# Performance work log

Measured on AMD Instinct MI355X. Metric: run time of the kernel, lower is better.

The kernel has to match this reference:

```python
import jax, jax.numpy as jnp
import numpy as np

SOFTCAP = 15.0
EPS_RMS = 1e-6
EPS_L2 = 1e-12


def rms_norm(x):
    # F.rms_norm without affine weight
    return x * jax.lax.rsqrt(jnp.mean(x * x, axis=-1, keepdims=True) + EPS_RMS)


def l2_normalize(x):
    # F.normalize(dim=-1): x / max(||x||, eps)
    n = jnp.sqrt(jnp.sum(x * x, axis=-1, keepdims=True))
    return x / jnp.maximum(n, EPS_L2)


def setup_inputs() -> dict:
    key = jax.random.key(0)
    ks = jax.random.split(key, 7)
    B, D, H, KVH, HD = 2, 1024, 16, 4, 64
    chunk_start_idx, chunk_len, n_scratchpad = 2048, 2048, 64
    T = chunk_start_idx + chunk_len + n_scratchpad  # 4160
    s = 0.02
    return {
        "x": jax.random.normal(ks[0], (B, T, D), dtype=jnp.float32),
        "Wq": jax.random.normal(ks[1], (D, D), dtype=jnp.float32) * s,
        "Wk": jax.random.normal(ks[2], (KVH * HD, D), dtype=jnp.float32) * s,
        "Wv": jax.random.normal(ks[3], (KVH * HD, D), dtype=jnp.float32) * s,
        "Wo": jax.random.normal(ks[4], (D, D), dtype=jnp.float32) * s,
        "Wfc": jax.random.normal(ks[5], (4 * D, D), dtype=jnp.float32) * s,
        "Wproj": jax.random.normal(ks[6], (D, 4 * D), dtype=jnp.float32) * s,
        "chunk_start_idx": chunk_start_idx,
        "chunk_len": chunk_len,
        "n_scratchpad": n_scratchpad,
    }


def reference(x, Wq, Wk, Wv, Wo, Wfc, Wproj, chunk_start_idx, chunk_len, n_scratchpad):
    B, T, D = x.shape
    H = 16
    KVH = Wk.shape[0] // (D // H)
    HD = D // H
    update_start = chunk_start_idx
    n_update = T - update_start

    x_norm = rms_norm(x)
    x_upd = x_norm[:, update_start:]

    q = (x_upd @ Wq.T).reshape(B, n_update, H, HD).transpose(0, 2, 1, 3)   # [B,H,Q,hd]
    k = (x_norm @ Wk.T).reshape(B, T, KVH, HD).transpose(0, 2, 1, 3)       # [B,KVH,T,hd]
    v = (x_norm @ Wv.T).reshape(B, T, KVH, HD).transpose(0, 2, 1, 3)

    q = l2_normalize(q)
    k = l2_normalize(k)

    if KVH < H:
        rep = H // KVH
        k = jnp.repeat(k, rep, axis=1)
        v = jnp.repeat(v, rep, axis=1)

    scale = 1.0 / jnp.sqrt(jnp.float32(HD))
    scores = jnp.einsum("bhqd,bhkd->bhqk", q, k) * scale
    q_pos = jnp.arange(update_start, T)[:, None]
    kv_pos = jnp.arange(T)[None, :]
    mask = kv_pos <= q_pos  # [Q,T] causal
    scores = jnp.where(mask[None, None], scores, -jnp.inf)
    probs = jax.nn.softmax(scores, axis=-1)
    attn = jnp.einsum("bhqk,bhkd->bhqd", probs, v)             # [B,H,Q,hd]
    attn = attn.transpose(0, 2, 1, 3).reshape(B, n_update, D)

    attn_out = attn @ Wo.T
    attn_out = SOFTCAP * jnp.tanh(attn_out / SOFTCAP)

    x_new = x[:, update_start:] + attn_out
    h = rms_norm(x_new) @ Wfc.T
    h = jnp.square(jax.nn.relu(h))  # nanochat MLP: relu(x)^2
    x_new = x_new + h @ Wproj.T

    if update_start > 0:
        return jnp.concatenate([x[:, :update_start], x_new], axis=1)
    return x_new
```

## Files before the change

kernel.cpp:

```cpp
#include <hip/hip_runtime.h>
#include <hip/hip_bf16.h>

#define B_   2
#define T_   4160
#define D_   1024
#define H_   16
#define KVH_ 4
#define HD_  64
#define UPD  2048
#define NU   2112
#define MQ   (B_*NU)
#define MT   (B_*T_)

typedef unsigned short u16;
typedef unsigned int u32;
typedef __attribute__((ext_vector_type(8))) short bf16x8;
typedef __attribute__((ext_vector_type(4))) float f32x4;
typedef __attribute__((ext_vector_type(4))) unsigned short u16x4;

__device__ __forceinline__ float bf2f(u16 u){ return __uint_as_float(((unsigned)u)<<16); }
__device__ __forceinline__ u16 f2bf(float f){
  unsigned u = __float_as_uint(f);
  u += 0x7FFF + ((u>>16)&1);
  return (u16)(u>>16);
}

__device__ __forceinline__ void gll16(const void* g, void* l){
  __builtin_amdgcn_global_load_lds((const __attribute__((address_space(1))) char*)g,
                                   (__attribute__((address_space(3))) char*)l, 16, 0, 0);
}

template<int N> __device__ __forceinline__ void wait_vm(){
  if constexpr(N==0) asm volatile("s_waitcnt vmcnt(0)" ::: "memory");
  else if constexpr(N==3) asm volatile("s_waitcnt vmcnt(3)" ::: "memory");
  else if constexpr(N==4) asm volatile("s_waitcnt vmcnt(4)" ::: "memory");
}

__global__ void cast_all(const float* __restrict__ s0, const float* __restrict__ s1,
                         const float* __restrict__ s2, const float* __restrict__ s3,
                         const float* __restrict__ s4, const float* __restrict__ s5,
                         u16* __restrict__ d0, u16* __restrict__ d1, u16* __restrict__ d2,
                         u16* __restrict__ d3, u16* __restrict__ d4, u16* __restrict__ d5){
  int blk = blockIdx.x;
  const float* s; u16* d; int base;
  if      (blk < 1024){ s=s0; d=d0; base=blk; }
  else if (blk < 1280){ s=s1; d=d1; base=blk-1024; }
  else if (blk < 1536){ s=s2; d=d2; base=blk-1280; }
  else if (blk < 2560){ s=s3; d=d3; base=blk-1536; }
  else if (blk < 6656){ s=s4; d=d4; base=blk-2560; }
  else                { s=s5; d=d5; base=blk-6656; }
  int i = base*256 + threadIdx.x;
  float4 v = ((const float4*)s)[i];
  u16x4 u; u.x=f2bf(v.x); u.y=f2bf(v.y); u.z=f2bf(v.z); u.w=f2bf(v.w);
  ((u16x4*)d)[i] = u;
}

__global__ void rmsnorm_kernel(const float* __restrict__ in, u16* __restrict__ obf,
                               float* __restrict__ copy_out, int withcopy){
  int row = blockIdx.x;
  int t = threadIdx.x;
  const float* xr = in + (size_t)row*D_;
  float4 v = ((const float4*)xr)[t];
  float ss = v.x*v.x + v.y*v.y + v.z*v.z + v.w*v.w;
  #pragma unroll
  for (int o=32;o;o>>=1) ss += __shfl_xor(ss, o);
  __shared__ float red[4];
  if ((t&63)==0) red[t>>6] = ss;
  __syncthreads();
  float tot = red[0]+red[1]+red[2]+red[3];
  float sc = rsqrtf(tot*(1.0f/D_) + 1e-6f);
  u16x4 o4; o4.x=f2bf(v.x*sc); o4.y=f2bf(v.y*sc); o4.z=f2bf(v.z*sc); o4.w=f2bf(v.w*sc);
  ((u16x4*)(obf + (size_t)row*D_))[t] = o4;
  if (withcopy && (row % T_) < UPD)
    ((float4*)(copy_out + (size_t)row*D_))[t] = v;
}

__global__ void l2norm_kernel(u16* __restrict__ buf, int nvec, float scale){
  int vid = blockIdx.x*4 + (threadIdx.x>>6);
  int ln = threadIdx.x & 63;
  if (vid >= nvec) return;
  u16* p = buf + (size_t)vid*64 + ln;
  float x = bf2f(*p);
  float ss = x*x;
  #pragma unroll
  for (int o=32;o;o>>=1) ss += __shfl_xor(ss, o);
  float n = sqrtf(ss);
  n = (n < 1e-12f) ? 1e-12f : n;
  *p = f2bf(x * scale / n);
}

template<int EPI, int AMAP, int BN>
__global__ __launch_bounds__(256) void gemm_bt(
    const u16* __restrict__ A, const u16* __restrict__ Bw, void* __restrict__ C,
    void* __restrict__ aux, int M, int N, int K)
{
  constexpr int MI = (BN==128) ? 4 : 2;
  constexpr int NB = BN/64;
  __shared__ alignas(16) u16 sA[3][4096];
  __shared__ alignas(16) u16 sB[3][BN*32];
  unsigned nwg = gridDim.x*gridDim.y;
  unsigned flat = blockIdx.y*gridDim.x + blockIdx.x;
  unsigned nf = (flat&7)*(nwg>>3) + (flat>>3);
  int m0 = (int)(nf / gridDim.x) * 128;
  int n0 = (int)(nf % gridDim.x) * BN;
  int tid = threadIdx.x;
  int wv = tid>>6, ln = tid&63;
  int wr = (BN==128) ? (wv>>1) : wv;
  int wc = (BN==128) ? (wv&1)  : 0;
  int lr = ln&15, lg = ln>>4;

  const char* pA[2]; int dA[2];
  #pragma unroll
  for (int c=0;c<2;c++){
    int ci = c*256 + tid;
    int row = ci>>2, csw = (ci&3) ^ (row&3);
    int arow = m0 + row;
    if (AMAP==1) arow = (arow/NU)*T_ + UPD + (arow%NU);
    pA[c] = (const char*)A + ((size_t)arow*K + csw*8)*2;
    dA[c] = (c*256 + wv*64)*16;
  }
  const char* pB[NB]; int dB[NB];
  #pragma unroll
  for (int c=0;c<NB;c++){
    int ci = c*256 + tid;
    int row = ci>>2, csw = (ci&3) ^ (row&3);
    pB[c] = (const char*)Bw + ((size_t)(n0+row)*K + csw*8)*2;
    dB[c] = (c*256 + wv*64)*16;
  }

  auto stage = [&](int bu, int kt){
    #pragma unroll
    for (int c=0;c<2;c++)  gll16(pA[c] + kt*64, (char*)sA[bu] + dA[c]);
    #pragma unroll
    for (int c=0;c<NB;c++) gll16(pB[c] + kt*64, (char*)sB[bu] + dB[c]);
  };

  f32x4 acc[MI][4] = {};
  int nk = K>>5;
  stage(0,0); stage(1,1);
  for (int t=0; t<nk; ++t){
    int bu = t%3;
    if (t+1<nk) wait_vm<2+NB>(); else wait_vm<0>();
    __builtin_amdgcn_s_barrier();
    __builtin_amdgcn_sched_barrier(0);
    if (t+2<nk) stage((t+2)%3, t+2);
    bf16x8 af[MI], bfr[4];
    #pragma unroll
    for (int i=0;i<MI;i++){
      int row = wr*(MI*16) + i*16 + lr;
      af[i] = *(const bf16x8*)&sA[bu][row*32 + (lg ^ (lr&3))*8];
    }
    #pragma unroll
    for (int j=0;j<4;j++){
      int row = wc*64 + j*16 + lr;
      bfr[j] = *(const bf16x8*)&sB[bu][row*32 + (lg ^ (lr&3))*8];
    }
    #pragma unroll
    for (int i=0;i<MI;i++)
      #pragma unroll
      for (int j=0;j<4;j++)
        acc[i][j] = __builtin_amdgcn_mfma_f32_16x16x32_bf16(af[i], bfr[j], acc[i][j], 0,0,0);
  }
  #pragma unroll
  for (int i=0;i<MI;i++)
    #pragma unroll
    for (int j=0;j<4;j++){
      int grow0 = m0 + wr*(MI*16) + i*16 + lg*4;
      int gcol  = n0 + wc*64 + j*16 + lr;
      if (EPI==5){
        if (gcol < 256){
          #pragma unroll
          for (int r=0;r<4;r++)
            ((u16*)C)[(size_t)(grow0+r)*256 + gcol] = f2bf(acc[i][j][r]);
        } else {
          int bb = grow0 / T_;
          int t  = grow0 - bb*T_;
          int kvh = (gcol>>6)&3, d = gcol&63;
          u16x4 pk;
          #pragma unroll
          for (int r=0;r<4;r++) pk[r] = f2bf(acc[i][j][r]);
          *(u16x4*)((u16*)aux + ((size_t)((bb*KVH_+kvh)*64 + d))*T_ + t) = pk;
        }
      } else {
        #pragma unroll
        for (int r=0;r<4;r++){
          int grow = grow0 + r;
          float cv = acc[i][j][r];
          if (EPI==0){
            ((u16*)C)[(size_t)grow*N + gcol] = f2bf(cv);
          } else if (EPI==1){
            int b = grow/NU, t = grow - b*NU;
            float e = __expf(cv*(2.0f/15.0f));
            float val = 15.f*(e-1.f)/(e+1.f) + ((const float*)aux)[((size_t)(b*T_ + UPD + t))*D_ + gcol];
            ((float*)C)[(size_t)grow*N + gcol] = val;
          } else if (EPI==2){
            float rr = cv>0.f ? cv : 0.f;
            ((u16*)C)[(size_t)grow*N + gcol] = f2bf(rr*rr);
          } else {
            int b = grow/NU, t = grow - b*NU;
            float val = ((const float*)aux)[(size_t)grow*N + gcol] + cv;
            ((float*)C)[((size_t)(b*T_ + UPD + t))*D_ + gcol] = val;
          }
        }
      }
    }
}

template<bool DIAG>
__device__ __forceinline__ void sm_pack(const f32x4 (&s)[2][4], char* spw,
                                        int lr, int lg, int ktb, int qbg){
  #pragma unroll
  for (int qi=0;qi<2;qi++)
    #pragma unroll
    for (int k2=0;k2<4;k2++){
      float p[4];
      #pragma unroll
      for (int r=0;r<4;r++){
        float pv = __builtin_amdgcn_exp2f(s[qi][k2][r]);
        if (DIAG){
          int kpos = ktb + k2*16 + lg*4 + r;
          int qpos = qbg + qi*16 + lr;
          if (kpos > qpos) pv = 0.f;
        }
        p[r] = pv;
      }
      __hip_bfloat162 w0 = __float22bfloat162_rn(float2{p[0],p[1]});
      __hip_bfloat162 w1 = __float22bfloat162_rn(float2{p[2],p[3]});
      uint2 wd; wd.x = *(u32*)&w0; wd.y = *(u32*)&w1;
      *(uint2*)(spw + (qi*16+lr)*128 + ((k2*32 + lg*8) ^ ((lr&7)<<4))) = wd;
    }
}

__global__ __launch_bounds__(256) void attn_kernel(
    const u16* __restrict__ qb, const u16* __restrict__ kb,
    const u16* __restrict__ vT, u16* __restrict__ ab)
{
  __shared__ alignas(16) u16 sK[3][64*64];
  __shared__ alignas(16) u16 sV[3][64*64];
  __shared__ alignas(16) u16 sP[4][32*64];
  unsigned flat = (blockIdx.z*4u + blockIdx.y)*66u + blockIdx.x;
  unsigned nf = (flat&7)*66u + (flat>>3);
  int qi_blk = 65 - (int)(nf % 66u);
  unsigned khb = nf / 66u;
  int kh = (int)(khb & 3), b = (int)(khb >> 2);
  int tid = threadIdx.x, wv = tid>>6, ln = tid&63;
  int lr = ln&15, lg = ln>>4;
  int h = kh*4 + wv;
  int qrow0 = qi_blk*32;
  int qbg = UPD + qrow0;
  char* spw = (char*)&sP[wv][0];

  bf16x8 qf[2][2];
  #pragma unroll
  for (int qi=0;qi<2;qi++){
    const u16* qp = qb + (size_t)(b*NU + qrow0 + qi*16 + lr)*D_ + h*HD_;
    qf[qi][0] = *(const bf16x8*)(qp + lg*8);
    qf[qi][1] = *(const bf16x8*)(qp + 32 + lg*8);
  }
  bf16x8 ones;
  #pragma unroll
  for (int i=0;i<8;i++) ones[i] = (short)0x3F80;

  f32x4 accO[2][4] = {};
  f32x4 accD[2] = {};

  const char* pK[2]; const char* pV[2]; int dst[2];
  #pragma unroll
  for (int cc=0; cc<2; ++cc){
    int ci = cc*256 + tid;
    int row = ci>>3, slotb = (ci&7)*16;
    int scolb = slotb ^ ((row&7)<<4);
    pK[cc] = (const char*)kb + ((size_t)(b*T_ + row)*256 + kh*HD_)*2 + scolb;
    pV[cc] = (const char*)vT + ((size_t)((b*KVH_+kh)*64 + row)*T_)*2 + scolb;
    dst[cc] = (cc*256 + wv*64)*16;
  }
  auto stage = [&](int bu, int kt){
    #pragma unroll
    for (int cc=0; cc<2; ++cc)
      gll16(pK[cc] + kt*32768, (char*)sK[bu] + dst[cc]);
    #pragma unroll
    for (int cc=0; cc<2; ++cc)
      gll16(pV[cc] + kt*128,   (char*)sV[bu] + dst[cc]);
  };

  int nkt = 33 + (qi_blk>>1);
  stage(0,0); stage(1,1);
  for (int kt=0; kt<nkt; ++kt){
    int bu = kt%3;
    if (kt+1<nkt) wait_vm<4>(); else wait_vm<0>();
    __builtin_amdgcn_s_barrier();
    __builtin_amdgcn_sched_barrier(0);
    if (kt+2<nkt) stage((kt+2)%3, kt+2);
    f32x4 s[2][4];
    #pragma unroll
    for (int qi=0;qi<2;qi++)
      #pragma unroll
      for (int k2=0;k2<4;k2++) s[qi][k2] = (f32x4){0.f,0.f,0.f,0.f};
    #pragma unroll
    for (int k2=0;k2<4;k2++){
      int row = k2*16 + lr;
      int sw = (row&7)<<4;
      bf16x8 k0 = *(const bf16x8*)((const char*)sK[bu] + row*128 + ((lg*16)^sw));
      bf16x8 k1 = *(const bf16x8*)((const char*)sK[bu] + row*128 + ((64+lg*16)^sw));
      #pragma unroll
      for (int qi=0;qi<2;qi++){
        s[qi][k2] = __builtin_amdgcn_mfma_f32_16x16x32_bf16(k0, qf[qi][0], s[qi][k2], 0,0,0);
        s[qi][k2] = __builtin_amdgcn_mfma_f32_16x16x32_bf16(k1, qf[qi][1], s[qi][k2], 0,0,0);
      }
    }
    if (kt+1 < nkt) sm_pack<false>(s, spw, lr, lg, kt*64, qbg);
    else            sm_pack<true >(s, spw, lr, lg, kt*64, qbg);
    bf16x8 pf[2][2];
    #pragma unroll
    for (int qi=0;qi<2;qi++)
      #pragma unroll
      for (int hf=0;hf<2;hf++)
        pf[qi][hf] = *(const bf16x8*)(spw + (qi*16+lr)*128 + ((hf*64 + lg*16) ^ ((lr&7)<<4)));
    #pragma unroll
    for (int dt=0; dt<4; ++dt){
      int row = dt*16 + lr;
      int sw = (row&7)<<4;
      bf16x8 v0 = *(const bf16x8*)((const char*)sV[bu] + row*128 + ((lg*16)^sw));
      bf16x8 v1 = *(const bf16x8*)((const char*)sV[bu] + row*128 + ((64+lg*16)^sw));
      #pragma unroll
      for (int qi=0;qi<2;qi++){
        accO[qi][dt] = __builtin_amdgcn_mfma_f32_16x16x32_bf16(pf[qi][0], v0, accO[qi][dt], 0,0,0);
        accO[qi][dt] = __builtin_amdgcn_mfma_f32_16x16x32_bf16(pf[qi][1], v1, accO[qi][dt], 0,0,0);
      }
    }
    #pragma unroll
    for (int qi=0;qi<2;qi++){
      accD[qi] = __builtin_amdgcn_mfma_f32_16x16x32_bf16(pf[qi][0], ones, accD[qi], 0,0,0);
      accD[qi] = __builtin_amdgcn_mfma_f32_16x16x32_bf16(pf[qi][1], ones, accD[qi], 0,0,0);
    }
  }
  #pragma unroll
  for (int qi=0;qi<2;qi++)
    #pragma unroll
    for (int dt=0; dt<4; ++dt)
      #pragma unroll
      for (int r=0;r<4;r++){
        float val = accO[qi][dt][r] / accD[qi][r];
        size_t row = (size_t)(b*NU + qrow0 + qi*16 + lg*4 + r);
        ab[row*D_ + h*HD_ + dt*16 + lr] = f2bf(val);
      }
}

extern "C" void kernel_launch(void* const* d_in, const int* in_sizes, int n_in,
                              void* d_out, int out_size, void* d_ws, size_t ws_size,
                              hipStream_t stream)
{
  const float* x     = (const float*)d_in[0];
  const float* Wq    = (const float*)d_in[1];
  const float* Wk    = (const float*)d_in[2];
  const float* Wv    = (const float*)d_in[3];
  const float* Wo    = (const float*)d_in[4];
  const float* Wfc   = (const float*)d_in[5];
  const float* Wproj = (const float*)d_in[6];
  float* out = (float*)d_out;

  char* ws = (char*)d_ws;
  size_t off = 0;
  auto alloc = [&](size_t bytes)->char*{ char* p = ws + off; off += (bytes + 255) & ~(size_t)255; return p; };
  u16* wqb  = (u16*)alloc((size_t)D_*D_*2);
  u16* wkvb = (u16*)alloc((size_t)512*D_*2);
  u16* wob  = (u16*)alloc((size_t)D_*D_*2);
  u16* wfcb = (u16*)alloc((size_t)4096*D_*2);
  u16* wpb  = (u16*)alloc((size_t)D_*4096*2);
  u16* xn   = (u16*)alloc((size_t)MT*D_*2);
  u16* qB   = (u16*)alloc((size_t)MQ*D_*2);
  u16* kB   = (u16*)alloc((size_t)MT*256*2);
  u16* vTb  = (u16*)alloc((size_t)B_*KVH_*64*T_*2);
  u16* aB   = (u16*)alloc((size_t)MQ*D_*2);
  float* xnew = (float*)alloc((size_t)MQ*D_*4);
  u16* xn2  = (u16*)alloc((size_t)MQ*D_*2);
  u16* hB   = (u16*)alloc((size_t)MQ*4096*2);
  (void)ws_size; (void)in_sizes; (void)n_in; (void)out_size;

  cast_all<<<10752, 256, 0, stream>>>(Wq, Wk, Wv, Wo, Wfc, Wproj,
                                      wqb, wkvb, wkvb + (size_t)256*D_, wob, wfcb, wpb);

  rmsnorm_kernel<<<MT, 256, 0, stream>>>(x, xn, out, 1);

  gemm_bt<0,1,64><<<dim3(16,33), 256, 0, stream>>>(xn, wqb, qB, nullptr, MQ, D_,  D_);
  gemm_bt<5,0,64><<<dim3(8,65),  256, 0, stream>>>(xn, wkvb, kB, vTb, MT, 512, D_);

  l2norm_kernel<<<(MQ*H_)/4, 256, 0, stream>>>(qB, MQ*H_, 1.0f);
  l2norm_kernel<<<(MT*KVH_)/4, 256, 0, stream>>>(kB, MT*KVH_, 0.18033688f);

  attn_kernel<<<dim3(66,4,2), 256, 0, stream>>>(qB, kB, vTb, aB);

  gemm_bt<1,0,64><<<dim3(16,33), 256, 0, stream>>>(aB, wob, xnew, (void*)x, MQ, D_, D_);

  rmsnorm_kernel<<<MQ, 256, 0, stream>>>(xnew, xn2, nullptr, 0);
  gemm_bt<2,0,128><<<dim3(32,33), 256, 0, stream>>>(xn2, wfcb, hB, nullptr, MQ, 4096, D_);
  gemm_bt<3,0,64><<<dim3(16,33), 256, 0, stream>>>(hB, wpb, out, xnew, MQ, D_, 4096);
}
```

Baseline: 454.6 us.

## Stage GEMM epilogues through LDS for coalesced stores; double-buffer attention loads

The GEMM epilogue now writes accumulators into shared memory (reusing the staging buffers), then reads them back so each thread issues 16-byte coalesced row stores. This also vectorizes the fp32 residual and softcap epilogues with float4 reads of the aux tensor. Separately, the attention kernel drops from triple to double buffering, using __syncthreads in place of explicit vmcnt waits. That lowers LDS use, but the loads now have less time to overlap compute and each iteration pays a full barrier.

```diff
diff --git a/kernel.cpp b/kernel.cpp
--- a/kernel.cpp
+++ b/kernel.cpp
@@ -96,8 +96,7 @@
 {
   constexpr int MI = (BN==128) ? 4 : 2;
   constexpr int NB = BN/64;
-  __shared__ alignas(16) u16 sA[3][4096];
-  __shared__ alignas(16) u16 sB[3][BN*32];
+  __shared__ alignas(16) u16 smem[3*4096 + 3*(BN*32)];
   unsigned nwg = gridDim.x*gridDim.y;
   unsigned flat = blockIdx.y*gridDim.x + blockIdx.x;
   unsigned nf = (flat&7)*(nwg>>3) + (flat>>3);
@@ -128,11 +127,14 @@
     dB[c] = (c*256 + wv*64)*16;
   }
 
+  auto sAb = [&](int bu)->u16*{ return smem + bu*4096; };
+  auto sBb = [&](int bu)->u16*{ return smem + 3*4096 + bu*(BN*32); };
+
   auto stage = [&](int bu, int kt){
     #pragma unroll
-    for (int c=0;c<2;c++)  gll16(pA[c] + kt*64, (char*)sA[bu] + dA[c]);
-    #pragma unroll
-    for (int c=0;c<NB;c++) gll16(pB[c] + kt*64, (char*)sB[bu] + dB[c]);
+    for (int c=0;c<2;c++)  gll16(pA[c] + kt*64, (char*)sAb(bu) + dA[c]);
+    #pragma unroll
+    for (int c=0;c<NB;c++) gll16(pB[c] + kt*64, (char*)sBb(bu) + dB[c]);
   };
 
   f32x4 acc[MI][4] = {};
@@ -148,12 +150,12 @@
     #pragma unroll
     for (int i=0;i<MI;i++){
       int row = wr*(MI*16) + i*16 + lr;
-      af[i] = *(const bf16x8*)&sA[bu][row*32 + (lg ^ (lr&3))*8];
+      af[i] = *(const bf16x8*)&sAb(bu)[row*32 + (lg ^ (lr&3))*8];
     }
     #pragma unroll
     for (int j=0;j<4;j++){
       int row = wc*64 + j*16 + lr;
-      bfr[j] = *(const bf16x8*)&sB[bu][row*32 + (lg ^ (lr&3))*8];
+      bfr[j] = *(const bf16x8*)&sBb(bu)[row*32 + (lg ^ (lr&3))*8];
     }
     #pragma unroll
     for (int i=0;i<MI;i++)
@@ -161,13 +163,14 @@
       for (int j=0;j<4;j++)
         acc[i][j] = __builtin_amdgcn_mfma_f32_16x16x32_bf16(af[i], bfr[j], acc[i][j], 0,0,0);
   }
-  #pragma unroll
-  for (int i=0;i<MI;i++)
-    #pragma unroll
-    for (int j=0;j<4;j++){
-      int grow0 = m0 + wr*(MI*16) + i*16 + lg*4;
-      int gcol  = n0 + wc*64 + j*16 + lr;
-      if (EPI==5){
+
+  if (EPI==5){
+    #pragma unroll
+    for (int i=0;i<MI;i++)
+      #pragma unroll
+      for (int j=0;j<4;j++){
+        int grow0 = m0 + wr*(MI*16) + i*16 + lg*4;
+        int gcol  = n0 + wc*64 + j*16 + lr;
         if (gcol < 256){
           #pragma unroll
           for (int r=0;r<4;r++)
@@ -181,29 +184,70 @@
           for (int r=0;r<4;r++) pk[r] = f2bf(acc[i][j][r]);
           *(u16x4*)((u16*)aux + ((size_t)((bb*KVH_+kvh)*64 + d))*T_ + t) = pk;
         }
-      } else {
+      }
+  } else if (EPI==0 || EPI==2){
+    __syncthreads();
+    u16* sE = smem;
+    #pragma unroll
+    for (int i=0;i<MI;i++)
+      #pragma unroll
+      for (int j=0;j<4;j++)
         #pragma unroll
         for (int r=0;r<4;r++){
-          int grow = grow0 + r;
           float cv = acc[i][j][r];
-          if (EPI==0){
-            ((u16*)C)[(size_t)grow*N + gcol] = f2bf(cv);
-          } else if (EPI==1){
-            int b = grow/NU, t = grow - b*NU;
-            float e = __expf(cv*(2.0f/15.0f));
-            float val = 15.f*(e-1.f)/(e+1.f) + ((const float*)aux)[((size_t)(b*T_ + UPD + t))*D_ + gcol];
-            ((float*)C)[(size_t)grow*N + gcol] = val;
-          } else if (EPI==2){
-            float rr = cv>0.f ? cv : 0.f;
-            ((u16*)C)[(size_t)grow*N + gcol] = f2bf(rr*rr);
-          } else {
-            int b = grow/NU, t = grow - b*NU;
-            float val = ((const float*)aux)[(size_t)grow*N + gcol] + cv;
-            ((float*)C)[((size_t)(b*T_ + UPD + t))*D_ + gcol] = val;
-          }
+          if (EPI==2){ float rr = cv>0.f ? cv : 0.f; cv = rr*rr; }
+          sE[(wr*(MI*16)+i*16+lg*4+r)*BN + wc*64 + j*16 + lr] = f2bf(cv);
         }
-      }
-    }
+    if (BN==64){
+      #pragma unroll
+      for (int p=0;p<4;p++){
+        int rl = wv*32 + p*8 + (ln>>3);
+        int cb = (ln&7)*8;
+        bf16x8 v = *(const bf16x8*)&sE[rl*64 + cb];
+        *(bf16x8*)&((u16*)C)[(size_t)(m0+rl)*N + n0 + cb] = v;
+      }
+    } else {
+      __syncthreads();
+      #pragma unroll
+      for (int p=0;p<8;p++){
+        int rl = p*16 + (tid>>4);
+        int cb = (tid&15)*8;
+        bf16x8 v = *(const bf16x8*)&sE[rl*128 + cb];
+        *(bf16x8*)&((u16*)C)[(size_t)(m0+rl)*N + n0 + cb] = v;
+      }
+    }
+  } else {
+    __syncthreads();
+    float* sF = (float*)smem;
+    #pragma unroll
+    for (int i=0;i<MI;i++)
+      #pragma unroll
+      for (int j=0;j<4;j++)
+        #pragma unroll
+        for (int r=0;r<4;r++)
+          sF[(wr*32+i*16+lg*4+r)*64 + j*16 + lr] = acc[i][j][r];
+    #pragma unroll
+    for (int p=0;p<8;p++){
+      int rl = wv*32 + p*4 + (ln>>4);
+      int c4 = (ln&15)*4;
+      float4 v = *(const float4*)&sF[rl*64 + c4];
+      int grow = m0 + rl;
+      int b = grow/NU, t = grow - b*NU;
+      if (EPI==1){
+        const float4 ax = *(const float4*)&((const float*)aux)[((size_t)(b*T_+UPD+t))*D_ + n0 + c4];
+        float4 o;
+        { float e=__expf(v.x*(2.0f/15.0f)); o.x = 15.f*(e-1.f)/(e+1.f) + ax.x; }
+        { float e=__expf(v.y*(2.0f/15.0f)); o.y = 15.f*(e-1.f)/(e+1.f) + ax.y; }
+        { float e=__expf(v.z*(2.0f/15.0f)); o.z = 15.f*(e-1.f)/(e+1.f) + ax.z; }
+        { float e=__expf(v.w*(2.0f/15.0f)); o.w = 15.f*(e-1.f)/(e+1.f) + ax.w; }
+        *(float4*)&((float*)C)[(size_t)grow*N + n0 + c4] = o;
+      } else {
+        const float4 ax = *(const float4*)&((const float*)aux)[(size_t)grow*N + n0 + c4];
+        float4 o; o.x=v.x+ax.x; o.y=v.y+ax.y; o.z=v.z+ax.z; o.w=v.w+ax.w;
+        *(float4*)&((float*)C)[((size_t)(b*T_+UPD+t))*D_ + n0 + c4] = o;
+      }
+    }
+  }
 }
 
 template<bool DIAG>
@@ -235,9 +279,9 @@
     const u16* __restrict__ qb, const u16* __restrict__ kb,
     const u16* __restrict__ vT, u16* __restrict__ ab)
 {
-  __shared__ alignas(16) u16 sK[3][64*64];
-  __shared__ alignas(16) u16 sV[3][64*64];
-  __shared__ alignas(16) u16 sP[4][32*64];
+  __shared__ alignas(16) u16 sK[2][4096];
+  __shared__ alignas(16) u16 sV[2][4096];
+  __shared__ alignas(16) u16 sP[4][2048];
   unsigned flat = (blockIdx.z*4u + blockIdx.y)*66u + blockIdx.x;
   unsigned nf = (flat&7)*66u + (flat>>3);
   int qi_blk = 65 - (int)(nf % 66u);
@@ -284,13 +328,11 @@
   };
 
   int nkt = 33 + (qi_blk>>1);
-  stage(0,0); stage(1,1);
+  stage(0,0);
+  __syncthreads();
   for (int kt=0; kt<nkt; ++kt){
-    int bu = kt%3;
-    if (kt+1<nkt) wait_vm<4>(); else wait_vm<0>();
-    __builtin_amdgcn_s_barrier();
-    __builtin_amdgcn_sched_barrier(0);
-    if (kt+2<nkt) stage((kt+2)%3, kt+2);
+    int bu = kt&1;
+    if (kt+1 < nkt) stage(bu^1, kt+1);
     f32x4 s[2][4];
     #pragma unroll
     for (int qi=0;qi<2;qi++)
@@ -333,6 +375,7 @@
       accD[qi] = __builtin_amdgcn_mfma_f32_16x16x32_bf16(pf[qi][0], ones, accD[qi], 0,0,0);
       accD[qi] = __builtin_amdgcn_mfma_f32_16x16x32_bf16(pf[qi][1], ones, accD[qi], 0,0,0);
     }
+    __syncthreads();
   }
   #pragma unroll
   for (int qi=0;qi<2;qi++)
```

Result: no change. 455.5 us (+0.2%).
